# Optimization experiments

Hardware: AMD Instinct MI355X
Metric: run time of the kernel (lower is better)

## Reference

```python
import jax, jax.numpy as jnp
import numpy as np

N_FP = 235336   # n_fingerprint
N_WORD = 7844   # n_word
D = 10          # embed / hidden dim (hard-coded in module)
K = 23          # conv kernel 2*11+1
PAD = 11
N_ATOMS = 4096
L_WORDS = 65536


def setup_inputs() -> dict:
    key = jax.random.key(0)
    ks = jax.random.split(key, 16)
    s = 0.1  # weight init scale
    return {
        "fingerprints": jax.random.randint(ks[0], (N_ATOMS,), 0, N_FP),
        # scale adjacency so x + A@hs stays O(1) over 3 layers
        "adjacency": jax.random.uniform(ks[1], (N_ATOMS, N_ATOMS), dtype=jnp.float32) * (1.0 / N_ATOMS),
        "words": jax.random.randint(ks[2], (L_WORDS,), 0, N_WORD),
        "embed_fp": jax.random.normal(ks[3], (N_FP, D), dtype=jnp.float32) * s,
        "embed_word": jax.random.normal(ks[4], (N_WORD, D), dtype=jnp.float32) * s,
        "W_gnn_w": jax.random.normal(ks[5], (3, D, D), dtype=jnp.float32) * s,
        "W_gnn_b": jax.random.normal(ks[6], (3, D), dtype=jnp.float32) * s,
        "W_cnn_w": jax.random.normal(ks[7], (3, 1, 1, K, K), dtype=jnp.float32) * (s / K),
        "W_cnn_b": jax.random.normal(ks[8], (3,), dtype=jnp.float32) * s,
        "W_att_w": jax.random.normal(ks[9], (D, D), dtype=jnp.float32) * s,
        "W_att_b": jax.random.normal(ks[10], (D,), dtype=jnp.float32) * s,
        "W_out_w": jax.random.normal(ks[11], (3, 2 * D, 2 * D), dtype=jnp.float32) * s,
        "W_out_b": jax.random.normal(ks[12], (3, 2 * D), dtype=jnp.float32) * s,
        "W_int_w": jax.random.normal(ks[13], (2, 2 * D), dtype=jnp.float32) * s,
        "W_int_b": jax.random.normal(ks[14], (2,), dtype=jnp.float32) * s,
    }


def reference(fingerprints, adjacency, words, embed_fp, embed_word,
              W_gnn_w, W_gnn_b, W_cnn_w, W_cnn_b, W_att_w, W_att_b,
              W_out_w, W_out_b, W_int_w, W_int_b):
    # ---- Compound vector with GNN ----
    xs = embed_fp[fingerprints]                       # [N, D]
    for i in range(3):                                # fixed 3 layers
        hs = jax.nn.relu(xs @ W_gnn_w[i].T + W_gnn_b[i])
        xs = xs + adjacency @ hs                      # dense message passing
    compound = jnp.mean(xs, axis=0, keepdims=True)    # [1, D]

    # ---- Protein vector with attention-CNN ----
    ws = embed_word[words]                            # [L, D]
    t = ws[None, None]                                # [1,1,L,D] NCHW
    for i in range(3):
        t = jax.nn.relu(
            jax.lax.conv_general_dilated(t, W_cnn_w[i], (1, 1),
                                          [(PAD, PAD), (PAD, PAD)])
            + W_cnn_b[i])
    xs_p = t[0, 0]                                    # [L, D]

    h = jax.nn.relu(compound @ W_att_w.T + W_att_b)   # [1, D]
    hs_p = jax.nn.relu(xs_p @ W_att_w.T + W_att_b)    # [L, D]
    weights = jnp.tanh(h @ hs_p.T)                    # [1, L]
    ys = weights.T * hs_p                             # [L, D]
    protein = jnp.mean(ys, axis=0, keepdims=True)     # [1, D]

    # ---- Fusion MLP ----
    cat = jnp.concatenate([compound, protein], axis=1)  # [1, 2D]
    for j in range(3):
        cat = jax.nn.relu(cat @ W_out_w[j].T + W_out_b[j])
    return cat @ W_int_w.T + W_int_b                  # [1, 2]
```

## Files before the change

### kernel.cpp

```cpp
#include <hip/hip_runtime.h>
#include <hip/hip_bf16.h>
#include <math.h>

#define N_ATOMS 4096
#define L_WORDS 65536
#define DD 10
#define HALO 11

#define CONV_BLOCKS 256
#define CONV_BLOCK 256
#define GNN_BLOCKS 512
#define RPW 8
#define RPB 32
#define QCOLS 1024

__global__ __launch_bounds__(256) void gnn_embed(
    const int* __restrict__ fp, const float* __restrict__ embed_fp,
    float* __restrict__ xs0)
{
    int n = blockIdx.x * blockDim.x + threadIdx.x;
    if (n >= N_ATOMS) return;
    const float* e = embed_fp + (size_t)fp[n] * DD;
    #pragma unroll
    for (int d = 0; d < DD; ++d) xs0[n * DD + d] = e[d];
}

__global__ __launch_bounds__(256, 3) void fused_layer(
    const float* __restrict__ A,
    const float* __restrict__ xs0,
    const float* __restrict__ p0,
    const float* __restrict__ p1,
    float* __restrict__ part,
    const float* __restrict__ Wg, const float* __restrict__ bg,
    const float* __restrict__ tin, const int* __restrict__ words,
    const float* __restrict__ embed_word, const float* __restrict__ w,
    const float* __restrict__ bptr, float* __restrict__ tout)
{
    __shared__ float sh[DD * QCOLS];
    const int tid = threadIdx.x;

    if (blockIdx.x < CONV_BLOCKS) {
        float* s = sh;
        const int l0 = blockIdx.x * CONV_BLOCK;
        for (int idx = tid; idx < (CONV_BLOCK + 2 * HALO) * DD; idx += CONV_BLOCK) {
            int rr = idx / DD, d = idx - rr * DD;
            int gr = l0 - HALO + rr;
            float v = 0.f;
            if (gr >= 0 && gr < L_WORDS) {
                if (tin) v = tin[(size_t)gr * DD + d];
                else     v = embed_word[(size_t)words[gr] * DD + d];
            }
            s[rr * 11 + d] = v;
        }
        __syncthreads();

        const float bias = *bptr;
        float acc[DD];
        #pragma unroll
        for (int d = 0; d < DD; ++d) acc[d] = bias;
        for (int i = 0; i < 23; ++i) {
            float row[DD];
            const float* sr = &s[(tid + i) * 11];
            #pragma unroll
            for (int c = 0; c < DD; ++c) row[c] = sr[c];
            #pragma unroll
            for (int d = 0; d < DD; ++d) {
                #pragma unroll
                for (int c = 0; c < DD; ++c)
                    acc[d] += row[c] * w[i * 23 + (c - d + 11)];
            }
        }
        const int l = l0 + tid;
        #pragma unroll
        for (int d = 0; d < DD; ++d)
            tout[(size_t)l * DD + d] = fmaxf(acc[d], 0.f);
    } else {
        const int b = blockIdx.x - CONV_BLOCKS;
        const int wave = tid >> 6, lane = tid & 63;
        const int q = b & 3, rg = b >> 2;
        const int qbase = q * QCOLS;

        for (int j = 0; j < 4; ++j) {
            const int lc = j * 256 + tid;
            const int n = qbase + lc;
            float x[DD];
            #pragma unroll
            for (int d = 0; d < DD; ++d) x[d] = xs0[n * DD + d];
            if (p0) {
                #pragma unroll
                for (int qq = 0; qq < 4; ++qq)
                    #pragma unroll
                    for (int d = 0; d < DD; ++d)
                        x[d] += p0[((size_t)qq * N_ATOMS + n) * DD + d];
            }
            if (p1) {
                #pragma unroll
                for (int qq = 0; qq < 4; ++qq)
                    #pragma unroll
                    for (int d = 0; d < DD; ++d)
                        x[d] += p1[((size_t)qq * N_ATOMS + n) * DD + d];
            }
            #pragma unroll
            for (int d = 0; d < DD; ++d) {
                float v = bg[d];
                #pragma unroll
                for (int k = 0; k < DD; ++k) v += Wg[d * DD + k] * x[k];
                sh[d * QCOLS + lc] = fmaxf(v, 0.f);
            }
        }
        __syncthreads();

        const int r0 = rg * RPB + wave * RPW;
        const float4* A4 = (const float4*)(A + (size_t)r0 * N_ATOMS) + q * (QCOLS / 4);
        const float4* sh4 = (const float4*)sh;

        float acc[RPW][DD];
        #pragma unroll
        for (int r = 0; r < RPW; ++r)
            #pragma unroll
            for (int d = 0; d < DD; ++d) acc[r][d] = 0.f;

        #pragma unroll 1
        for (int it = 0; it < 4; ++it) {
            const int cb = it * 64 + lane;
            float4 a[RPW];
            #pragma unroll
            for (int r = 0; r < RPW; ++r) a[r] = A4[r * (N_ATOMS / 4) + cb];
            #pragma unroll
            for (int d = 0; d < DD; ++d) {
                float4 h = sh4[d * 256 + cb];
                #pragma unroll
                for (int r = 0; r < RPW; ++r) {
                    acc[r][d] += a[r].x * h.x;
                    acc[r][d] += a[r].y * h.y;
                    acc[r][d] += a[r].z * h.z;
                    acc[r][d] += a[r].w * h.w;
                }
            }
        }

        #pragma unroll
        for (int m = 1; m <= 4; m <<= 1) {
            #pragma unroll
            for (int r = 0; r < RPW; ++r)
                #pragma unroll
                for (int d = 0; d < DD; ++d)
                    acc[r][d] += __shfl_xor(acc[r][d], m, 64);
        }
        __syncthreads();

        if ((lane & 7) == 0) {
            const int g = lane >> 3;
            float* dst = &sh[(wave * 8 + g) * 80];
            #pragma unroll
            for (int r = 0; r < RPW; ++r)
                #pragma unroll
                for (int d = 0; d < DD; ++d) dst[r * DD + d] = acc[r][d];
        }
        __syncthreads();

        float* pdst = part + ((size_t)q * N_ATOMS + rg * RPB) * DD;
        for (int o = tid; o < RPB * DD; o += 256) {
            const int w8 = o / 80;
            const int k = o - w8 * 80;
            float v = 0.f;
            #pragma unroll
            for (int g = 0; g < 8; ++g) v += sh[(w8 * 8 + g) * 80 + k];
            pdst[o] = v;
        }
    }
}

__global__ __launch_bounds__(256) void comp_reduce(
    const float* __restrict__ xs0, const float* __restrict__ p0,
    const float* __restrict__ p1, const float* __restrict__ p2,
    float* __restrict__ comp_part)
{
    const int tid = threadIdx.x, wave = tid >> 6, lane = tid & 63;
    const int n = blockIdx.x * 256 + tid;
    float x[DD];
    #pragma unroll
    for (int d = 0; d < DD; ++d) {
        float v = xs0[n * DD + d];
        #pragma unroll
        for (int qq = 0; qq < 4; ++qq) {
            v += p0[((size_t)qq * N_ATOMS + n) * DD + d];
            v += p1[((size_t)qq * N_ATOMS + n) * DD + d];
            v += p2[((size_t)qq * N_ATOMS + n) * DD + d];
        }
        x[d] = v;
    }
    #pragma unroll
    for (int m = 32; m >= 1; m >>= 1) {
        #pragma unroll
        for (int d = 0; d < DD; ++d) x[d] += __shfl_xor(x[d], m, 64);
    }
    __shared__ float s[4][DD];
    if (lane == 0) {
        #pragma unroll
        for (int d = 0; d < DD; ++d) s[wave][d] = x[d];
    }
    __syncthreads();
    if (tid < DD)
        comp_part[blockIdx.x * DD + tid] =
            s[0][tid] + s[1][tid] + s[2][tid] + s[3][tid];
}

__global__ __launch_bounds__(1024) void attention_pool(
    const float* __restrict__ xs_p, const float* __restrict__ comp_part,
    const float* __restrict__ Wa, const float* __restrict__ ba,
    float* __restrict__ att_part)
{
    __shared__ float shc[DD];
    __shared__ float s[16][DD];
    const int tid = threadIdx.x, wave = tid >> 6, lane = tid & 63;
    const int l = blockIdx.x * 1024 + tid;

    if (tid < DD) {
        float c = 0.f;
        #pragma unroll
        for (int p = 0; p < 16; ++p) c += comp_part[p * DD + tid];
        shc[tid] = c * (1.f / N_ATOMS);
    }
    __syncthreads();

    float h[DD];
    #pragma unroll
    for (int d = 0; d < DD; ++d) {
        float v = ba[d];
        #pragma unroll
        for (int k = 0; k < DD; ++k) v += Wa[d * DD + k] * shc[k];
        h[d] = fmaxf(v, 0.f);
    }

    float row[DD];
    #pragma unroll
    for (int d = 0; d < DD; ++d) row[d] = xs_p[(size_t)l * DD + d];

    float hp[DD], dotv = 0.f;
    #pragma unroll
    for (int d = 0; d < DD; ++d) {
        float v = ba[d];
        #pragma unroll
        for (int k = 0; k < DD; ++k) v += Wa[d * DD + k] * row[k];
        hp[d] = fmaxf(v, 0.f);
        dotv += h[d] * hp[d];
    }
    const float wgt = tanhf(dotv);

    float y[DD];
    #pragma unroll
    for (int d = 0; d < DD; ++d) y[d] = wgt * hp[d];
    #pragma unroll
    for (int m = 32; m >= 1; m >>= 1) {
        #pragma unroll
        for (int d = 0; d < DD; ++d) y[d] += __shfl_xor(y[d], m, 64);
    }
    if (lane == 0) {
        #pragma unroll
        for (int d = 0; d < DD; ++d) s[wave][d] = y[d];
    }
    __syncthreads();
    if (tid < DD) {
        float v = 0.f;
        #pragma unroll
        for (int wv = 0; wv < 16; ++wv) v += s[wv][tid];
        att_part[blockIdx.x * DD + tid] = v;
    }
}

__global__ __launch_bounds__(64) void final_mlp(
    const float* __restrict__ comp_part, const float* __restrict__ att_part,
    const float* __restrict__ Wo, const float* __restrict__ bo,
    const float* __restrict__ Wi, const float* __restrict__ bi,
    float* __restrict__ out)
{
    const int t = threadIdx.x;
    float a[DD];
    #pragma unroll
    for (int d = 0; d < DD; ++d) a[d] = att_part[t * DD + d];
    #pragma unroll
    for (int m = 32; m >= 1; m >>= 1) {
        #pragma unroll
        for (int d = 0; d < DD; ++d) a[d] += __shfl_xor(a[d], m, 64);
    }
    __shared__ float cat[20];
    if (t < DD) {
        float c = 0.f;
        #pragma unroll
        for (int p = 0; p < 16; ++p) c += comp_part[p * DD + t];
        cat[t] = c * (1.f / N_ATOMS);
    }
    if (t == 0) {
        #pragma unroll
        for (int d = 0; d < DD; ++d) cat[DD + d] = a[d] * (1.f / L_WORDS);
    }
    __syncthreads();
    for (int j = 0; j < 3; ++j) {
        float v = 0.f;
        if (t < 20) {
            v = bo[j * 20 + t];
            for (int k = 0; k < 20; ++k) v += Wo[j * 400 + t * 20 + k] * cat[k];
        }
        __syncthreads();
        if (t < 20) cat[t] = fmaxf(v, 0.f);
        __syncthreads();
    }
    if (t < 2) {
        float v = bi[t];
        for (int k = 0; k < 20; ++k) v += Wi[t * 20 + k] * cat[k];
        out[t] = v;
    }
}

extern "C" void kernel_launch(void* const* d_in, const int* in_sizes, int n_in,
                              void* d_out, int out_size, void* d_ws, size_t ws_size,
                              hipStream_t stream)
{
    const int*   fp     = (const int*)d_in[0];
    const float* A      = (const float*)d_in[1];
    const int*   words  = (const int*)d_in[2];
    const float* emb_fp = (const float*)d_in[3];
    const float* emb_w  = (const float*)d_in[4];
    const float* Wg     = (const float*)d_in[5];
    const float* bg     = (const float*)d_in[6];
    const float* Wc     = (const float*)d_in[7];
    const float* bc     = (const float*)d_in[8];
    const float* Wa     = (const float*)d_in[9];
    const float* ba     = (const float*)d_in[10];
    const float* Wo     = (const float*)d_in[11];
    const float* bo     = (const float*)d_in[12];
    const float* Wi     = (const float*)d_in[13];
    const float* bi     = (const float*)d_in[14];
    float* out = (float*)d_out;
    float* ws  = (float*)d_ws;

    float* xs0   = ws;
    float* ta    = ws + 40960;
    float* tb    = ws + 696320;
    float* part0 = ws + 1351680;
    float* part1 = ws + 1515520;
    float* part2 = ws + 1679360;
    float* comp_part = ws + 1843200;
    float* att_part  = ws + 1843456;

    const int fused_grid = CONV_BLOCKS + GNN_BLOCKS;

    gnn_embed<<<N_ATOMS / 256, 256, 0, stream>>>(fp, emb_fp, xs0);

    fused_layer<<<fused_grid, 256, 0, stream>>>(
        A, xs0, nullptr, nullptr, part0, Wg, bg,
        nullptr, words, emb_w, Wc, bc, ta);

    fused_layer<<<fused_grid, 256, 0, stream>>>(
        A, xs0, part0, nullptr, part1, Wg + 100, bg + 10,
        ta, nullptr, nullptr, Wc + 529, bc + 1, tb);

    fused_layer<<<fused_grid, 256, 0, stream>>>(
        A, xs0, part0, part1, part2, Wg + 200, bg + 20,
        tb, nullptr, nullptr, Wc + 1058, bc + 2, ta);

    comp_reduce<<<16, 256, 0, stream>>>(xs0, part0, part1, part2, comp_part);

    attention_pool<<<L_WORDS / 1024, 1024, 0, stream>>>(
        ta, comp_part, Wa, ba, att_part);

    final_mlp<<<1, 64, 0, stream>>>(comp_part, att_part, Wo, bo, Wi, bi, out);
}
```

Measured before the change: 205.8 us.

## Hoist GNN hidden-state compute into separate prep kernels with d-major layout

Before, each of the 512 GNN blocks recomputed the layer update (xs plus all previous partials, then the 10x10 linear and ReLU) for its quarter of the atoms, which duplicated the work across row groups. Now small gnn_embed/gnn_prep kernels compute xs and hs once per layer and store them d-major. fused_layer just copies hs into shared memory with float4 loads, and the partial outputs move to d-major as well. The cost is two extra kernel launches between layers, which adds serial launch gaps.

```diff
diff --git a/kernel.cpp b/kernel.cpp
--- a/kernel.cpp
+++ b/kernel.cpp
@@ -1,5 +1,4 @@
 #include <hip/hip_runtime.h>
-#include <hip/hip_bf16.h>
 #include <math.h>
 
 #define N_ATOMS 4096
@@ -14,24 +13,56 @@
 #define RPB 32
 #define QCOLS 1024
 
-__global__ __launch_bounds__(256) void gnn_embed(
+__global__ __launch_bounds__(128) void gnn_embed(
     const int* __restrict__ fp, const float* __restrict__ embed_fp,
-    float* __restrict__ xs0)
-{
-    int n = blockIdx.x * blockDim.x + threadIdx.x;
-    if (n >= N_ATOMS) return;
+    const float* __restrict__ Wg, const float* __restrict__ bg,
+    float* __restrict__ xs, float* __restrict__ hs)
+{
+    const int n = blockIdx.x * 128 + threadIdx.x;
+    float x[DD];
     const float* e = embed_fp + (size_t)fp[n] * DD;
     #pragma unroll
-    for (int d = 0; d < DD; ++d) xs0[n * DD + d] = e[d];
+    for (int d = 0; d < DD; ++d) x[d] = e[d];
+    #pragma unroll
+    for (int d = 0; d < DD; ++d) xs[d * N_ATOMS + n] = x[d];
+    #pragma unroll
+    for (int d = 0; d < DD; ++d) {
+        float v = bg[d];
+        #pragma unroll
+        for (int k = 0; k < DD; ++k) v += Wg[d * DD + k] * x[k];
+        hs[d * N_ATOMS + n] = fmaxf(v, 0.f);
+    }
+}
+
+__global__ __launch_bounds__(128) void gnn_prep(
+    const float* __restrict__ xs_in, const float* __restrict__ part,
+    const float* __restrict__ Wg, const float* __restrict__ bg,
+    float* __restrict__ xs_out, float* __restrict__ hs)
+{
+    const int n = blockIdx.x * 128 + threadIdx.x;
+    float x[DD];
+    #pragma unroll
+    for (int d = 0; d < DD; ++d) {
+        float v = xs_in[d * N_ATOMS + n];
+        #pragma unroll
+        for (int q = 0; q < 4; ++q)
+            v += part[((size_t)q * DD + d) * N_ATOMS + n];
+        x[d] = v;
+        xs_out[d * N_ATOMS + n] = v;
+    }
+    #pragma unroll
+    for (int d = 0; d < DD; ++d) {
+        float v = bg[d];
+        #pragma unroll
+        for (int k = 0; k < DD; ++k) v += Wg[d * DD + k] * x[k];
+        hs[d * N_ATOMS + n] = fmaxf(v, 0.f);
+    }
 }
 
 __global__ __launch_bounds__(256, 3) void fused_layer(
     const float* __restrict__ A,
-    const float* __restrict__ xs0,
-    const float* __restrict__ p0,
-    const float* __restrict__ p1,
+    const float* __restrict__ hs,
     float* __restrict__ part,
-    const float* __restrict__ Wg, const float* __restrict__ bg,
     const float* __restrict__ tin, const int* __restrict__ words,
     const float* __restrict__ embed_word, const float* __restrict__ w,
     const float* __restrict__ bptr, float* __restrict__ tout)
@@ -78,36 +109,12 @@
         const int b = blockIdx.x - CONV_BLOCKS;
         const int wave = tid >> 6, lane = tid & 63;
         const int q = b & 3, rg = b >> 2;
-        const int qbase = q * QCOLS;
-
-        for (int j = 0; j < 4; ++j) {
-            const int lc = j * 256 + tid;
-            const int n = qbase + lc;
-            float x[DD];
-            #pragma unroll
-            for (int d = 0; d < DD; ++d) x[d] = xs0[n * DD + d];
-            if (p0) {
-                #pragma unroll
-                for (int qq = 0; qq < 4; ++qq)
-                    #pragma unroll
-                    for (int d = 0; d < DD; ++d)
-                        x[d] += p0[((size_t)qq * N_ATOMS + n) * DD + d];
-            }
-            if (p1) {
-                #pragma unroll
-                for (int qq = 0; qq < 4; ++qq)
-                    #pragma unroll
-                    for (int d = 0; d < DD; ++d)
-                        x[d] += p1[((size_t)qq * N_ATOMS + n) * DD + d];
-            }
-            #pragma unroll
-            for (int d = 0; d < DD; ++d) {
-                float v = bg[d];
-                #pragma unroll
-                for (int k = 0; k < DD; ++k) v += Wg[d * DD + k] * x[k];
-                sh[d * QCOLS + lc] = fmaxf(v, 0.f);
-            }
-        }
+
+        const float4* h4 = (const float4*)hs;
+        float4* shw = (float4*)sh;
+        #pragma unroll
+        for (int d = 0; d < DD; ++d)
+            shw[d * 256 + tid] = h4[d * (N_ATOMS / 4) + q * 256 + tid];
         __syncthreads();
 
         const int r0 = rg * RPB + wave * RPW;
@@ -159,21 +166,20 @@
         }
         __syncthreads();
 
-        float* pdst = part + ((size_t)q * N_ATOMS + rg * RPB) * DD;
+        float* pdst = part + (size_t)q * DD * N_ATOMS + (size_t)rg * RPB;
         for (int o = tid; o < RPB * DD; o += 256) {
-            const int w8 = o / 80;
-            const int k = o - w8 * 80;
+            const int d = o >> 5, rr = o & 31;
+            const int w8 = rr >> 3, r = rr & 7;
             float v = 0.f;
             #pragma unroll
-            for (int g = 0; g < 8; ++g) v += sh[(w8 * 8 + g) * 80 + k];
-            pdst[o] = v;
+            for (int g = 0; g < 8; ++g) v += sh[(w8 * 8 + g) * 80 + r * DD + d];
+            pdst[d * N_ATOMS + rr] = v;
         }
     }
 }
 
 __global__ __launch_bounds__(256) void comp_reduce(
-    const float* __restrict__ xs0, const float* __restrict__ p0,
-    const float* __restrict__ p1, const float* __restrict__ p2,
+    const float* __restrict__ xs, const float* __restrict__ p2,
     float* __restrict__ comp_part)
 {
     const int tid = threadIdx.x, wave = tid >> 6, lane = tid & 63;
@@ -181,13 +187,10 @@
     float x[DD];
     #pragma unroll
     for (int d = 0; d < DD; ++d) {
-        float v = xs0[n * DD + d];
-        #pragma unroll
-        for (int qq = 0; qq < 4; ++qq) {
-            v += p0[((size_t)qq * N_ATOMS + n) * DD + d];
-            v += p1[((size_t)qq * N_ATOMS + n) * DD + d];
-            v += p2[((size_t)qq * N_ATOMS + n) * DD + d];
-        }
+        float v = xs[d * N_ATOMS + n];
+        #pragma unroll
+        for (int qq = 0; qq < 4; ++qq)
+            v += p2[((size_t)qq * DD + d) * N_ATOMS + n];
         x[d] = v;
     }
     #pragma unroll
@@ -336,31 +339,37 @@
     float* ws  = (float*)d_ws;
 
     float* xs0   = ws;
-    float* ta    = ws + 40960;
-    float* tb    = ws + 696320;
-    float* part0 = ws + 1351680;
-    float* part1 = ws + 1515520;
-    float* part2 = ws + 1679360;
-    float* comp_part = ws + 1843200;
-    float* att_part  = ws + 1843456;
+    float* xs1   = ws + 40960;
+    float* xs2   = ws + 81920;
+    float* hs    = ws + 122880;
+    float* ta    = ws + 163840;
+    float* tb    = ws + 819200;
+    float* part0 = ws + 1474560;
+    float* part1 = ws + 1638400;
+    float* part2 = ws + 1802240;
+    float* comp_part = ws + 1966080;
+    float* att_part  = ws + 1966240;
 
     const int fused_grid = CONV_BLOCKS + GNN_BLOCKS;
 
-    gnn_embed<<<N_ATOMS / 256, 256, 0, stream>>>(fp, emb_fp, xs0);
+    gnn_embed<<<N_ATOMS / 128, 128, 0, stream>>>(fp, emb_fp, Wg, bg, xs0, hs);
 
     fused_layer<<<fused_grid, 256, 0, stream>>>(
-        A, xs0, nullptr, nullptr, part0, Wg, bg,
-        nullptr, words, emb_w, Wc, bc, ta);
+        A, hs, part0, nullptr, words, emb_w, Wc, bc, ta);
+
+    gnn_prep<<<N_ATOMS / 128, 128, 0, stream>>>(
+        xs0, part0, Wg + 100, bg + 10, xs1, hs);
 
     fused_layer<<<fused_grid, 256, 0, stream>>>(
-        A, xs0, part0, nullptr, part1, Wg + 100, bg + 10,
-        ta, nullptr, nullptr, Wc + 529, bc + 1, tb);
+        A, hs, part1, ta, words, emb_w, Wc + 529, bc + 1, tb);
+
+    gnn_prep<<<N_ATOMS / 128, 128, 0, stream>>>(
+        xs1, part1, Wg + 200, bg + 20, xs2, hs);
 
     fused_layer<<<fused_grid, 256, 0, stream>>>(
-        A, xs0, part0, part1, part2, Wg + 200, bg + 20,
-        tb, nullptr, nullptr, Wc + 1058, bc + 2, ta);
-
-    comp_reduce<<<16, 256, 0, stream>>>(xs0, part0, part1, part2, comp_part);
+        A, hs, part2, tb, words, emb_w, Wc + 1058, bc + 2, ta);
+
+    comp_reduce<<<16, 256, 0, stream>>>(xs2, part2, comp_part);
 
     attention_pool<<<L_WORDS / 1024, 1024, 0, stream>>>(
         ta, comp_part, Wa, ba, att_part);
```

New measurement: 206.5 us. About the same (+0.3%).
